# Optimization experiments

Measured on AMD Instinct MI355X. Metric: run time of the kernel, lower is better.

Reference implementation:

```python
import jax, jax.numpy as jnp
import numpy as np

B, D, H, K = 32768, 784, 500, 50


def setup_inputs() -> dict:
    key = jax.random.key(0)
    ks = jax.random.split(key, 12)
    s = 0.02  # weight init scale
    return {
        "x": jax.random.uniform(ks[0], (B, D), dtype=jnp.float32),
        "u": jax.random.uniform(ks[1], (B, K), dtype=jnp.float32),
        "enc_w1": jax.random.normal(ks[2], (D, H), dtype=jnp.float32) * s,
        "enc_b1": jnp.zeros((H,), jnp.float32),
        "w_alpha": jax.random.normal(ks[3], (H, K), dtype=jnp.float32) * s,
        "b_alpha": jnp.zeros((K,), jnp.float32),
        "w_beta": jax.random.normal(ks[4], (H, K), dtype=jnp.float32) * s,
        "b_beta": jnp.zeros((K,), jnp.float32),
        "dec_w1": jax.random.normal(ks[5], (K, H), dtype=jnp.float32) * s,
        "dec_b1": jnp.zeros((H,), jnp.float32),
        "dec_w2": jax.random.normal(ks[6], (H, D), dtype=jnp.float32) * s,
        "dec_b2": jnp.zeros((D,), jnp.float32),
    }


def reference(x, u, enc_w1, enc_b1, w_alpha, b_alpha, w_beta, b_beta,
              dec_w1, dec_b1, dec_w2, dec_b2):
    # encode
    h = jax.nn.relu(x @ enc_w1 + enc_b1)                       # [B,H]
    alpha = jax.nn.softplus(h @ w_alpha + b_alpha)             # [B,K] > 0
    beta = jax.nn.softplus(h @ w_beta + b_beta)                # [B,K] > 0
    # Kumaraswamy inverse-CDF sample: v = (1 - u^(1/beta))^(1/alpha)
    v = (1.0 - u ** (1.0 / beta)) ** (1.0 / alpha)             # [B,K]
    # stick-breaking: pi[k] = v[k] * prod_{j<k}(1 - v[j])  (exclusive cumprod)
    cp = jnp.cumprod(1.0 - v, axis=-1)                         # [B,K]
    pi = v * jnp.concatenate([jnp.ones_like(v[:, :1]), cp[:, :-1]], axis=-1)
    # decode
    hd = jax.nn.relu(pi @ dec_w1 + dec_b1)                     # [B,H]
    recon_x = jax.nn.sigmoid(hd @ dec_w2 + dec_b2)             # [B,D]
    return recon_x, alpha, beta
```

## Files before the change

### kernel.cpp

```cpp
#include <hip/hip_runtime.h>
#include <math.h>


typedef __bf16 bf16x8 __attribute__((ext_vector_type(8)));
typedef float f32x4 __attribute__((ext_vector_type(4)));

#define BATCH 32768
#define BM 128
#define BN 128
#define BK 64
#define NTHR 512

__device__ __forceinline__ unsigned short bf16_bits(float f) {
    __bf16 b = (__bf16)f;
    return __builtin_bit_cast(unsigned short, b);
}

__device__ __forceinline__ void gll16(const unsigned short* src, unsigned short* ldsdst) {
    __builtin_amdgcn_global_load_lds(
        (const __attribute__((address_space(1))) unsigned int*)src,
        (__attribute__((address_space(3))) unsigned int*)ldsdst,
        16, 0, 0);
}

template<int MODE, bool AF32>
__global__ __launch_bounds__(NTHR, 4) void mfma_gemm(
    const void* __restrict__ Av,
    const unsigned short* __restrict__ Bt,
    const float* __restrict__ bias,
    void* __restrict__ Cv,
    int Kpad, int Kreal, int lda, int ldc, int Nreal, int nbx)
{
    __shared__ unsigned short As[BM * BK];
    __shared__ unsigned short Bs[BN * BK];

    const int nwg = gridDim.x;
    const int orig = blockIdx.x;
    const int q = nwg >> 3, r8 = nwg & 7;
    const int xcd = orig & 7;
    const int chunkbase = (xcd < r8) ? xcd * (q + 1) : r8 * (q + 1) + (xcd - r8) * q;
    const int wgid = chunkbase + (orig >> 3);
    const int bn = wgid % nbx;
    const size_t block_m = (size_t)(wgid / nbx) * BM;
    const int block_n = bn * BN;

    const int tid = threadIdx.x;
    const int l = tid & 63;
    const int wid = tid >> 6;
    const int wr = wid >> 2, wc = wid & 3;

    const int lr = l & 15;
    const int kh = l >> 4;

    f32x4 acc[4][2] = {};

    auto issueB = [&](int k0) {
        #pragma unroll
        for (int i = 0; i < 2; ++i) {
            int chunk = wid * 2 + i;
            int gid = chunk * 64 + l;
            int r = gid >> 3;
            int kgs = (gid & 7) ^ (r & 7);
            gll16(Bt + (size_t)(block_n + r) * Kpad + k0 + kgs * 8, Bs + chunk * 512);
        }
    };

    auto compute = [&]() {
        #pragma unroll
        for (int s = 0; s < 2; ++s) {
            bf16x8 af[4], bf[2];
            #pragma unroll
            for (int mi = 0; mi < 4; ++mi) {
                int row = wr * 64 + mi * 16 + lr;
                int g = (s * 4 + kh) ^ (row & 7);
                af[mi] = *(const bf16x8*)(As + row * 64 + g * 8);
            }
            #pragma unroll
            for (int ni = 0; ni < 2; ++ni) {
                int row = wc * 32 + ni * 16 + lr;
                int g = (s * 4 + kh) ^ (row & 7);
                bf[ni] = *(const bf16x8*)(Bs + row * 64 + g * 8);
            }
            #pragma unroll
            for (int mi = 0; mi < 4; ++mi)
                #pragma unroll
                for (int ni = 0; ni < 2; ++ni)
                    acc[mi][ni] = __builtin_amdgcn_mfma_f32_16x16x32_bf16(
                        af[mi], bf[ni], acc[mi][ni], 0, 0, 0);
        }
    };

    if constexpr (AF32) {
        const float* Af = (const float*)Av;
        float4 areg[4];
        bool aok[2];
        const int clampk = Kreal - 8;

        auto issueA = [&](int k0) {
            #pragma unroll
            for (int i = 0; i < 2; ++i) {
                int gid = i * NTHR + tid;
                int r = gid >> 3, kg = gid & 7;
                int gk = k0 + kg * 8;
                int gkc = (gk <= clampk) ? gk : clampk;
                const float4* p = (const float4*)(Af + (block_m + r) * (size_t)lda + gkc);
                areg[2 * i]     = p[0];
                areg[2 * i + 1] = p[1];
                aok[i] = (gk < Kreal);
            }
        };
        auto writeA = [&]() {
            #pragma unroll
            for (int i = 0; i < 2; ++i) {
                int gid = i * NTHR + tid;
                int r = gid >> 3, kg = gid & 7;
                union { __bf16 b[8]; uint4 u4; } pk;
                float4 f0 = areg[2 * i], f1 = areg[2 * i + 1];
                if (aok[i]) {
                    pk.b[0] = (__bf16)f0.x; pk.b[1] = (__bf16)f0.y;
                    pk.b[2] = (__bf16)f0.z; pk.b[3] = (__bf16)f0.w;
                    pk.b[4] = (__bf16)f1.x; pk.b[5] = (__bf16)f1.y;
                    pk.b[6] = (__bf16)f1.z; pk.b[7] = (__bf16)f1.w;
                } else {
                    pk.u4 = make_uint4(0, 0, 0, 0);
                }
                *(uint4*)(As + r * 64 + ((kg ^ (r & 7)) * 8)) = pk.u4;
            }
        };

        const int nt = Kpad / BK;
        issueA(0);
        for (int t = 0; t < nt - 1; ++t) {
            issueB(t * BK);
            writeA();
            issueA((t + 1) * BK);
            asm volatile("s_waitcnt vmcnt(4) lgkmcnt(0)" ::: "memory");
            __builtin_amdgcn_sched_barrier(0);
            __builtin_amdgcn_s_barrier();
            compute();
            __builtin_amdgcn_s_barrier();
        }
        issueB((nt - 1) * BK);
        writeA();
        asm volatile("s_waitcnt vmcnt(0) lgkmcnt(0)" ::: "memory");
        __builtin_amdgcn_sched_barrier(0);
        __builtin_amdgcn_s_barrier();
        compute();
    } else {
        const unsigned short* Ab = (const unsigned short*)Av;
        for (int k0 = 0; k0 < Kpad; k0 += BK) {
            issueB(k0);
            #pragma unroll
            for (int i = 0; i < 2; ++i) {
                int chunk = wid * 2 + i;
                int gid = chunk * 64 + l;
                int r = gid >> 3;
                int kgs = (gid & 7) ^ (r & 7);
                gll16(Ab + (block_m + r) * (size_t)lda + k0 + kgs * 8, As + chunk * 512);
            }
            __syncthreads();
            compute();
            __syncthreads();
        }
    }

    const int rg = (l >> 4) * 4;
    #pragma unroll
    for (int mi = 0; mi < 4; ++mi) {
        #pragma unroll
        for (int ni = 0; ni < 2; ++ni) {
            int gn = block_n + wc * 32 + ni * 16 + lr;
            float bs = bias[gn];
            #pragma unroll
            for (int j = 0; j < 4; ++j) {
                long gm = block_m + wr * 64 + mi * 16 + rg + j;
                float z = acc[mi][ni][j] + bs;
                if (MODE == 0) {
                    z = fmaxf(z, 0.f);
                    ((unsigned short*)Cv)[gm * ldc + gn] = bf16_bits(z);
                } else if (MODE == 1) {
                    z = (z > 0.f) ? z + __logf(1.f + __expf(-z))
                                  : __logf(1.f + __expf(z));
                    float* out = (float*)Cv;
                    if (gn < 50)       out[gm * 50 + gn] = z;
                    else if (gn < 100) out[(size_t)BATCH * 50 + gm * 50 + (gn - 50)] = z;
                } else {
                    if (gn < Nreal) {
                        z = __fdividef(1.f, 1.f + __expf(-z));
                        ((float*)Cv)[gm * Nreal + gn] = z;
                    }
                }
            }
        }
    }
}

__global__ __launch_bounds__(256) void prep_bt(
    const float* __restrict__ W, const float* __restrict__ bias,
    unsigned short* __restrict__ Bt, float* __restrict__ bpad,
    int Kr, int Nr, int Kpad, int Npad)
{
    int idx = blockIdx.x * 256 + threadIdx.x;
    if (idx >= Npad * Kpad) return;
    int n = idx / Kpad, k = idx - n * Kpad;
    float v = (n < Nr && k < Kr) ? W[(size_t)k * Nr + n] : 0.f;
    Bt[idx] = bf16_bits(v);
    if (k == 0) bpad[n] = (n < Nr) ? bias[n] : 0.f;
}

__global__ __launch_bounds__(256) void prep_wab(
    const float* __restrict__ Wa, const float* __restrict__ Wb,
    const float* __restrict__ ba, const float* __restrict__ bb,
    unsigned short* __restrict__ Bt, float* __restrict__ bpad)
{
    int idx = blockIdx.x * 256 + threadIdx.x;
    if (idx >= 128 * 512) return;
    int n = idx >> 9, k = idx & 511;
    float v = 0.f;
    if (k < 500) {
        if (n < 50)       v = Wa[(size_t)k * 50 + n];
        else if (n < 100) v = Wb[(size_t)k * 50 + (n - 50)];
    }
    Bt[idx] = bf16_bits(v);
    if (k == 0) bpad[n] = (n < 50) ? ba[n] : ((n < 100) ? bb[n - 50] : 0.f);
}

__global__ __launch_bounds__(256) void sample_pi(
    const float* __restrict__ u, const float* __restrict__ alpha,
    const float* __restrict__ beta, unsigned short* __restrict__ pib)
{
    int row = (blockIdx.x * 256 + threadIdx.x) >> 6;
    int lane = threadIdx.x & 63;
    size_t base = (size_t)row * 50;

    float v = 0.f, w = 1.f;
    if (lane < 50) {
        float a = alpha[base + lane];
        float b = beta[base + lane];
        float uu = u[base + lane];
        float t = exp2f(__fdividef(log2f(uu), b));
        v = exp2f(__fdividef(log2f(1.f - t), a));
        w = 1.f - v;
    }
    float p = w;
    #pragma unroll
    for (int off = 1; off < 64; off <<= 1) {
        float t = __shfl_up(p, off, 64);
        if (lane >= off) p *= t;
    }
    float ex = __shfl_up(p, 1, 64);
    if (lane == 0) ex = 1.f;
    float pi = v * ex;
    pib[(size_t)row * 64 + lane] = (lane < 50) ? bf16_bits(pi) : (unsigned short)0;
}

extern "C" void kernel_launch(void* const* d_in, const int* in_sizes, int n_in,
                              void* d_out, int out_size, void* d_ws, size_t ws_size,
                              hipStream_t stream) {
    const float* x       = (const float*)d_in[0];
    const float* u       = (const float*)d_in[1];
    const float* enc_w1  = (const float*)d_in[2];
    const float* enc_b1  = (const float*)d_in[3];
    const float* w_alpha = (const float*)d_in[4];
    const float* b_alpha = (const float*)d_in[5];
    const float* w_beta  = (const float*)d_in[6];
    const float* b_beta  = (const float*)d_in[7];
    const float* dec_w1  = (const float*)d_in[8];
    const float* dec_b1  = (const float*)d_in[9];
    const float* dec_w2  = (const float*)d_in[10];
    const float* dec_b2  = (const float*)d_in[11];

    const int D = 784;

    float* out   = (float*)d_out;
    float* recon = out;
    float* alpha = out + (size_t)BATCH * D;

    char* ws = (char*)d_ws;
    unsigned short* w1b  = (unsigned short*)(ws);
    unsigned short* wab  = (unsigned short*)(ws + 851968);
    unsigned short* dw1b = (unsigned short*)(ws + 983040);
    unsigned short* dw2b = (unsigned short*)(ws + 1048576);
    float* bias1  = (float*)(ws + 1966080);
    float* biasab = (float*)(ws + 1968128);
    float* biasd1 = (float*)(ws + 1970688);
    float* biasd2 = (float*)(ws + 1972736);
    unsigned short* h    = (unsigned short*)(ws + 2097152);
    unsigned short* pib  = (unsigned short*)(ws + 35651584);
    unsigned short* hdb  = h;

    prep_bt<<<dim3(512 * 832 / 256), 256, 0, stream>>>(
        enc_w1, enc_b1, w1b, bias1, 784, 500, 832, 512);
    prep_wab<<<dim3(256), 256, 0, stream>>>(w_alpha, w_beta, b_alpha, b_beta, wab, biasab);
    prep_bt<<<dim3(512 * 64 / 256), 256, 0, stream>>>(
        dec_w1, dec_b1, dw1b, biasd1, 50, 500, 64, 512);
    prep_bt<<<dim3(896 * 512 / 256), 256, 0, stream>>>(
        dec_w2, dec_b2, dw2b, biasd2, 500, 784, 512, 896);

    mfma_gemm<0, true><<<dim3((512 / BN) * (BATCH / BM)), NTHR, 0, stream>>>(
        x, w1b, bias1, h, 832, 784, 784, 512, 500, 512 / BN);

    mfma_gemm<1, false><<<dim3(BATCH / BM), NTHR, 0, stream>>>(
        h, wab, biasab, alpha, 512, 512, 512, 0, 100, 1);

    sample_pi<<<dim3(BATCH * 64 / 256), 256, 0, stream>>>(
        u, alpha, alpha + (size_t)BATCH * 50, pib);

    mfma_gemm<0, false><<<dim3((512 / BN) * (BATCH / BM)), NTHR, 0, stream>>>(
        pib, dw1b, biasd1, hdb, 64, 64, 64, 512, 500, 512 / BN);

    mfma_gemm<2, false><<<dim3((896 / BN) * (BATCH / BM)), NTHR, 0, stream>>>(
        hdb, dw2b, biasd2, recon, 512, 512, 512, 784, 784, 896 / BN);
}
```

Baseline: 145.3 us.

## Deepen prefetch pipeline in fp32-A GEMM with double-buffered B tile

In the fp32-input GEMM path (the first encoder layer), B tiles are now double-buffered in LDS and prefetched one step ahead. A tiles are held in two register sets loaded two K-steps ahead, with the waitcnt thresholds adjusted to match. The goal is to hide global-load latency behind the MFMA compute. In exchange it doubles B LDS usage for that path and adds register pressure, which could reduce occupancy.

After: 152.2 us. 1.05x slower.

```diff
diff --git a/kernel.cpp b/kernel.cpp
--- a/kernel.cpp
+++ b/kernel.cpp
@@ -31,8 +31,9 @@
     void* __restrict__ Cv,
     int Kpad, int Kreal, int lda, int ldc, int Nreal, int nbx)
 {
+    constexpr int NBSB = AF32 ? 2 : 1;
     __shared__ unsigned short As[BM * BK];
-    __shared__ unsigned short Bs[BN * BK];
+    __shared__ unsigned short Bs[NBSB * BN * BK];
 
     const int nwg = gridDim.x;
     const int orig = blockIdx.x;
@@ -54,18 +55,20 @@
 
     f32x4 acc[4][2] = {};
 
-    auto issueB = [&](int k0) {
+    auto issueB = [&](int k0, int buf) {
+        unsigned short* dst = Bs + buf * (BN * BK);
         #pragma unroll
         for (int i = 0; i < 2; ++i) {
             int chunk = wid * 2 + i;
             int gid = chunk * 64 + l;
             int r = gid >> 3;
             int kgs = (gid & 7) ^ (r & 7);
-            gll16(Bt + (size_t)(block_n + r) * Kpad + k0 + kgs * 8, Bs + chunk * 512);
+            gll16(Bt + (size_t)(block_n + r) * Kpad + k0 + kgs * 8, dst + chunk * 512);
         }
     };
 
-    auto compute = [&]() {
+    auto compute = [&](int buf) {
+        const unsigned short* bsrc = Bs + buf * (BN * BK);
         #pragma unroll
         for (int s = 0; s < 2; ++s) {
             bf16x8 af[4], bf[2];
@@ -79,7 +82,7 @@
             for (int ni = 0; ni < 2; ++ni) {
                 int row = wc * 32 + ni * 16 + lr;
                 int g = (s * 4 + kh) ^ (row & 7);
-                bf[ni] = *(const bf16x8*)(Bs + row * 64 + g * 8);
+                bf[ni] = *(const bf16x8*)(bsrc + row * 64 + g * 8);
             }
             #pragma unroll
             for (int mi = 0; mi < 4; ++mi)
@@ -90,13 +93,13 @@
         }
     };
 
+    const int nt = Kpad / BK;
+
     if constexpr (AF32) {
         const float* Af = (const float*)Av;
-        float4 areg[4];
-        bool aok[2];
         const int clampk = Kreal - 8;
 
-        auto issueA = [&](int k0) {
+        auto issueA = [&](int k0, float4 (&dst)[4]) {
             #pragma unroll
             for (int i = 0; i < 2; ++i) {
                 int gid = i * NTHR + tid;
@@ -104,19 +107,19 @@
                 int gk = k0 + kg * 8;
                 int gkc = (gk <= clampk) ? gk : clampk;
                 const float4* p = (const float4*)(Af + (block_m + r) * (size_t)lda + gkc);
-                areg[2 * i]     = p[0];
-                areg[2 * i + 1] = p[1];
-                aok[i] = (gk < Kreal);
+                dst[2 * i]     = p[0];
+                dst[2 * i + 1] = p[1];
             }
         };
-        auto writeA = [&]() {
+        auto writeA = [&](int t, const float4 (&src)[4]) {
             #pragma unroll
             for (int i = 0; i < 2; ++i) {
                 int gid = i * NTHR + tid;
                 int r = gid >> 3, kg = gid & 7;
+                int gk = t * BK + kg * 8;
                 union { __bf16 b[8]; uint4 u4; } pk;
-                float4 f0 = areg[2 * i], f1 = areg[2 * i + 1];
-                if (aok[i]) {
+                float4 f0 = src[2 * i], f1 = src[2 * i + 1];
+                if (gk < Kreal) {
                     pk.b[0] = (__bf16)f0.x; pk.b[1] = (__bf16)f0.y;
                     pk.b[2] = (__bf16)f0.z; pk.b[3] = (__bf16)f0.w;
                     pk.b[4] = (__bf16)f1.x; pk.b[5] = (__bf16)f1.y;
@@ -128,28 +131,42 @@
             }
         };
 
-        const int nt = Kpad / BK;
-        issueA(0);
-        for (int t = 0; t < nt - 1; ++t) {
-            issueB(t * BK);
-            writeA();
-            issueA((t + 1) * BK);
-            asm volatile("s_waitcnt vmcnt(4) lgkmcnt(0)" ::: "memory");
+        float4 aA[4], aB[4];
+        issueB(0, 0);
+        __builtin_amdgcn_sched_barrier(0);
+        issueA(0, aA);
+        issueA(BK, aB);
+        __builtin_amdgcn_sched_barrier(0);
+
+        auto step = [&](int t, float4 (&cur)[4]) {
+            const int buf = t & 1;
+            if (t + 1 < nt) issueB((t + 1) * BK, buf ^ 1);
+            __builtin_amdgcn_sched_barrier(0);
+            writeA(t, cur);
+            if (t + 2 < nt) issueA((t + 2) * BK, cur);
+            __builtin_amdgcn_sched_barrier(0);
+            if (t + 2 < nt) {
+                asm volatile("s_waitcnt vmcnt(10) lgkmcnt(0)" ::: "memory");
+            } else if (t + 1 < nt) {
+                asm volatile("s_waitcnt vmcnt(6) lgkmcnt(0)" ::: "memory");
+            } else {
+                asm volatile("s_waitcnt vmcnt(0) lgkmcnt(0)" ::: "memory");
+            }
             __builtin_amdgcn_sched_barrier(0);
             __builtin_amdgcn_s_barrier();
-            compute();
+            compute(buf);
             __builtin_amdgcn_s_barrier();
-        }
-        issueB((nt - 1) * BK);
-        writeA();
-        asm volatile("s_waitcnt vmcnt(0) lgkmcnt(0)" ::: "memory");
-        __builtin_amdgcn_sched_barrier(0);
-        __builtin_amdgcn_s_barrier();
-        compute();
+        };
+
+        for (int t = 0; t + 1 < nt; t += 2) {
+            step(t, aA);
+            step(t + 1, aB);
+        }
+        if (nt & 1) step(nt - 1, aA);
     } else {
         const unsigned short* Ab = (const unsigned short*)Av;
         for (int k0 = 0; k0 < Kpad; k0 += BK) {
-            issueB(k0);
+            issueB(k0, 0);
             #pragma unroll
             for (int i = 0; i < 2; ++i) {
                 int chunk = wid * 2 + i;
@@ -159,7 +176,7 @@
                 gll16(Ab + (block_m + r) * (size_t)lda + k0 + kgs * 8, As + chunk * 512);
             }
             __syncthreads();
-            compute();
+            compute(0);
             __syncthreads();
         }
     }
```

## Stream fp32 A tiles straight to LDS via global_load_lds, convert in compute

Applied to the files above, without the earlier changes.

The fp32-input GEMM path no longer loads A into registers, converts it to bf16 and writes it to LDS. It now uses direct global-to-LDS loads of the fp32 data into a doubled A buffer and converts to bf16 when reading fragments in the compute loop. Both paths share one simple load/sync/compute loop. This removes the VGPR staging and the LDS write instructions, but it drops the register-prefetch overlap. It also doubles the A LDS footprint, which may lower occupancy, and repeats the conversion across the waves that share the same A rows.

Result: slower. 260.7 us (+79.5%).

```diff
diff --git a/kernel.cpp b/kernel.cpp
--- a/kernel.cpp
+++ b/kernel.cpp
@@ -16,7 +16,7 @@
     return __builtin_bit_cast(unsigned short, b);
 }
 
-__device__ __forceinline__ void gll16(const unsigned short* src, unsigned short* ldsdst) {
+__device__ __forceinline__ void gll16(const void* src, void* ldsdst) {
     __builtin_amdgcn_global_load_lds(
         (const __attribute__((address_space(1))) unsigned int*)src,
         (__attribute__((address_space(3))) unsigned int*)ldsdst,
@@ -31,7 +31,7 @@
     void* __restrict__ Cv,
     int Kpad, int Kreal, int lda, int ldc, int Nreal, int nbx)
 {
-    __shared__ unsigned short As[BM * BK];
+    __shared__ unsigned char AsRaw[AF32 ? (BM * BK * 4) : (BM * BK * 2)];
     __shared__ unsigned short Bs[BN * BK];
 
     const int nwg = gridDim.x;
@@ -61,7 +61,39 @@
             int gid = chunk * 64 + l;
             int r = gid >> 3;
             int kgs = (gid & 7) ^ (r & 7);
-            gll16(Bt + (size_t)(block_n + r) * Kpad + k0 + kgs * 8, Bs + chunk * 512);
+            gll16(Bt + (size_t)(block_n + r) * Kpad + k0 + kgs * 8,
+                  (unsigned short*)Bs + chunk * 512);
+        }
+    };
+
+    auto issueA = [&](int k0) {
+        if constexpr (AF32) {
+            const float* Af = (const float*)Av;
+            const int clampA = Kreal - 4;
+            #pragma unroll
+            for (int i = 0; i < 4; ++i) {
+                int chunk = wid * 4 + i;
+                int gid = chunk * 64 + l;
+                int r = gid >> 4;
+                int gcol = gid & 15;
+                int p = gcol >> 1, half = gcol & 1;
+                int koff = (p ^ (r & 7)) * 8 + half * 4;
+                int gk = k0 + koff;
+                int gkc = (gk <= clampA) ? gk : clampA;
+                gll16(Af + (block_m + r) * (size_t)lda + gkc,
+                      AsRaw + chunk * 1024);
+            }
+        } else {
+            const unsigned short* Ab = (const unsigned short*)Av;
+            #pragma unroll
+            for (int i = 0; i < 2; ++i) {
+                int chunk = wid * 2 + i;
+                int gid = chunk * 64 + l;
+                int r = gid >> 3;
+                int kgs = (gid & 7) ^ (r & 7);
+                gll16(Ab + (block_m + r) * (size_t)lda + k0 + kgs * 8,
+                      (unsigned short*)AsRaw + chunk * 512);
+            }
         }
     };
 
@@ -72,14 +104,29 @@
             #pragma unroll
             for (int mi = 0; mi < 4; ++mi) {
                 int row = wr * 64 + mi * 16 + lr;
-                int g = (s * 4 + kh) ^ (row & 7);
-                af[mi] = *(const bf16x8*)(As + row * 64 + g * 8);
+                int j = (s * 4 + kh);
+                if constexpr (AF32) {
+                    const float* fp = (const float*)(AsRaw + row * 256 +
+                                                     ((j ^ (row & 7)) * 32));
+                    float4 q0 = ((const float4*)fp)[0];
+                    float4 q1 = ((const float4*)fp)[1];
+                    union { __bf16 b[8]; bf16x8 v; } cv;
+                    cv.b[0] = (__bf16)q0.x; cv.b[1] = (__bf16)q0.y;
+                    cv.b[2] = (__bf16)q0.z; cv.b[3] = (__bf16)q0.w;
+                    cv.b[4] = (__bf16)q1.x; cv.b[5] = (__bf16)q1.y;
+                    cv.b[6] = (__bf16)q1.z; cv.b[7] = (__bf16)q1.w;
+                    af[mi] = cv.v;
+                } else {
+                    int g = j ^ (row & 7);
+                    af[mi] = *(const bf16x8*)((const unsigned short*)AsRaw +
+                                              row * 64 + g * 8);
+                }
             }
             #pragma unroll
             for (int ni = 0; ni < 2; ++ni) {
                 int row = wc * 32 + ni * 16 + lr;
                 int g = (s * 4 + kh) ^ (row & 7);
-                bf[ni] = *(const bf16x8*)(Bs + row * 64 + g * 8);
+                bf[ni] = *(const bf16x8*)((const unsigned short*)Bs + row * 64 + g * 8);
             }
             #pragma unroll
             for (int mi = 0; mi < 4; ++mi)
@@ -90,78 +137,12 @@
         }
     };
 
-    if constexpr (AF32) {
-        const float* Af = (const float*)Av;
-        float4 areg[4];
-        bool aok[2];
-        const int clampk = Kreal - 8;
-
-        auto issueA = [&](int k0) {
-            #pragma unroll
-            for (int i = 0; i < 2; ++i) {
-                int gid = i * NTHR + tid;
-                int r = gid >> 3, kg = gid & 7;
-                int gk = k0 + kg * 8;
-                int gkc = (gk <= clampk) ? gk : clampk;
-                const float4* p = (const float4*)(Af + (block_m + r) * (size_t)lda + gkc);
-                areg[2 * i]     = p[0];
-                areg[2 * i + 1] = p[1];
-                aok[i] = (gk < Kreal);
-            }
-        };
-        auto writeA = [&]() {
-            #pragma unroll
-            for (int i = 0; i < 2; ++i) {
-                int gid = i * NTHR + tid;
-                int r = gid >> 3, kg = gid & 7;
-                union { __bf16 b[8]; uint4 u4; } pk;
-                float4 f0 = areg[2 * i], f1 = areg[2 * i + 1];
-                if (aok[i]) {
-                    pk.b[0] = (__bf16)f0.x; pk.b[1] = (__bf16)f0.y;
-                    pk.b[2] = (__bf16)f0.z; pk.b[3] = (__bf16)f0.w;
-                    pk.b[4] = (__bf16)f1.x; pk.b[5] = (__bf16)f1.y;
-                    pk.b[6] = (__bf16)f1.z; pk.b[7] = (__bf16)f1.w;
-                } else {
-                    pk.u4 = make_uint4(0, 0, 0, 0);
-                }
-                *(uint4*)(As + r * 64 + ((kg ^ (r & 7)) * 8)) = pk.u4;
-            }
-        };
-
-        const int nt = Kpad / BK;
-        issueA(0);
-        for (int t = 0; t < nt - 1; ++t) {
-            issueB(t * BK);
-            writeA();
-            issueA((t + 1) * BK);
-            asm volatile("s_waitcnt vmcnt(4) lgkmcnt(0)" ::: "memory");
-            __builtin_amdgcn_sched_barrier(0);
-            __builtin_amdgcn_s_barrier();
-            compute();
-            __builtin_amdgcn_s_barrier();
-        }
-        issueB((nt - 1) * BK);
-        writeA();
-        asm volatile("s_waitcnt vmcnt(0) lgkmcnt(0)" ::: "memory");
-        __builtin_amdgcn_sched_barrier(0);
-        __builtin_amdgcn_s_barrier();
+    for (int k0 = 0; k0 < Kpad; k0 += BK) {
+        issueB(k0);
+        issueA(k0);
+        __syncthreads();
         compute();
-    } else {
-        const unsigned short* Ab = (const unsigned short*)Av;
-        for (int k0 = 0; k0 < Kpad; k0 += BK) {
-            issueB(k0);
-            #pragma unroll
-            for (int i = 0; i < 2; ++i) {
-                int chunk = wid * 2 + i;
-                int gid = chunk * 64 + l;
-                int r = gid >> 3;
-                int kgs = (gid & 7) ^ (r & 7);
-                gll16(Ab + (block_m + r) * (size_t)lda + k0 + kgs * 8, As + chunk * 512);
-            }
-            __syncthreads();
-            compute();
-            __syncthreads();
-        }
+        __syncthreads();
     }
 
     const int rg = (l >> 4) * 4;
```
